# Kernel tuning notes

Measured on AMD Instinct MI355X. Metric: run time of the kernel, lower is better.

Reference implementation:

```python
import jax, jax.numpy as jnp
import numpy as np
import math

D_MODEL = 1024
N_HEADS = 16
D_HEAD = D_MODEL // N_HEADS


def setup_inputs() -> dict:
    key = jax.random.key(0)
    ks = jax.random.split(key, 9)
    B, S = 4, 2048
    scale = 1.0 / math.sqrt(D_MODEL)
    x = jax.random.normal(ks[0], (B, S, D_MODEL), dtype=jnp.float32)
    # nn.Linear weights stored as [out, in]; we keep [in, out] for x @ W
    w_q = jax.random.uniform(ks[1], (D_MODEL, D_MODEL), jnp.float32, -scale, scale)
    b_q = jax.random.uniform(ks[2], (D_MODEL,), jnp.float32, -scale, scale)
    w_k = jax.random.uniform(ks[3], (D_MODEL, D_MODEL), jnp.float32, -scale, scale)
    b_k = jax.random.uniform(ks[4], (D_MODEL,), jnp.float32, -scale, scale)
    w_v = jax.random.uniform(ks[5], (D_MODEL, D_MODEL), jnp.float32, -scale, scale)
    b_v = jax.random.uniform(ks[6], (D_MODEL,), jnp.float32, -scale, scale)
    w_o = jax.random.uniform(ks[7], (D_MODEL, D_MODEL), jnp.float32, -scale, scale)
    b_o = jax.random.uniform(ks[8], (D_MODEL,), jnp.float32, -scale, scale)
    return {"x": x, "w_q": w_q, "b_q": b_q, "w_k": w_k, "b_k": b_k,
            "w_v": w_v, "b_v": b_v, "w_o": w_o, "b_o": b_o}


def reference(x, w_q, b_q, w_k, b_k, w_v, b_v, w_o, b_o):
    B, S, _ = x.shape
    def split_heads(t):  # [B,S,D] -> [B,H,S,Dh]
        return t.reshape(B, S, N_HEADS, D_HEAD).transpose(0, 2, 1, 3)
    q = split_heads(x @ w_q + b_q)
    k = split_heads(x @ w_k + b_k)
    v = split_heads(x @ w_v + b_v)
    scores = jnp.einsum('bhqd,bhkd->bhqk', q, k) / math.sqrt(D_HEAD)
    attn = jax.nn.softmax(scores, axis=-1)  # dropout p=0 -> identity
    ctx = jnp.einsum('bhqk,bhkd->bhqd', attn, v)
    ctx = ctx.transpose(0, 2, 1, 3).reshape(B, S, D_MODEL)
    return ctx @ w_o + b_o
```

## Files before the change

kernel.cpp:

```cpp
#include <hip/hip_runtime.h>
#include <hip/hip_bf16.h>

#define DM   1024
#define SEQ  2048
#define NH   16
#define DH   64
#define BH   64
#define MTOT 8192

typedef __attribute__((ext_vector_type(8)))  short short8;
typedef __attribute__((ext_vector_type(4)))  short short4v;
typedef __attribute__((ext_vector_type(4)))  float f32x4;
typedef __attribute__((ext_vector_type(16))) float f32x16;
typedef __attribute__((ext_vector_type(4)))  float fvec4;
typedef __attribute__((ext_vector_type(4)))  int   i32x4;
typedef unsigned short ushort_t;

#define AS1 __attribute__((address_space(1)))
#define AS3 __attribute__((address_space(3)))

#define QSCALE 0.18033688011112042f
#define THR_L2 11.541560327111707f

static __device__ __forceinline__ unsigned short f2bf(float f){
  __bf16 h = (__bf16)f;
  return __builtin_bit_cast(unsigned short, h);
}

static __device__ __forceinline__ float fexp2(float x){
  float r;
  asm("v_exp_f32 %0, %1\n\ts_nop 0" : "=v"(r) : "v"(x));
  return r;
}

static __device__ __forceinline__ float fmax3(float a, float b, float c){
  float d;
  asm("v_max3_f32 %0, %1, %2, %3" : "=v"(d) : "v"(a), "v"(b), "v"(c));
  return d;
}

static __device__ __forceinline__ void gld16(const void* g, void* l){
  __builtin_amdgcn_global_load_lds((const AS1 int*)g, (AS3 int*)l, 16, 0, 0);
}

__global__ void k_cast_x(const float* __restrict__ x, ushort_t* __restrict__ xb){
  const size_t i = (size_t)blockIdx.x*256 + threadIdx.x;
  const fvec4* xv = (const fvec4*)x;
  fvec4 a = xv[2*i], b = xv[2*i+1];
  short8 r;
  #pragma unroll
  for (int j=0;j<4;++j) r[j]   = (short)f2bf(a[j]);
  #pragma unroll
  for (int j=0;j<4;++j) r[4+j] = (short)f2bf(b[j]);
  ((short8*)xb)[i] = r;
}

__global__ void k_cast_wt(const float* __restrict__ wq, const float* __restrict__ wk,
                          const float* __restrict__ wv, const float* __restrict__ wo,
                          ushort_t* __restrict__ wt){
  const int z = blockIdx.y;
  const float* W = (z==0)?wq:(z==1)?wk:(z==2)?wv:wo;
  ushort_t* Wt = wt + (size_t)z*DM*DM;
  const int k0 = (blockIdx.x & 15)*64, n0 = (blockIdx.x >> 4)*64;
  __shared__ float tile[64][65];
  const int t = threadIdx.x;
  #pragma unroll
  for (int it=0; it<4; ++it){
    int c = it*256 + t;
    int rr = c>>4, cc = c&15;
    fvec4 v = *(const fvec4*)(W + (size_t)(k0+rr)*DM + n0 + cc*4);
    #pragma unroll
    for (int j=0;j<4;++j) tile[cc*4+j][rr] = v[j];
  }
  __syncthreads();
  #pragma unroll
  for (int it=0; it<4; ++it){
    int c = it*256 + t;
    int nn = c>>4, kk = c&15;
    short4v r;
    #pragma unroll
    for (int j=0;j<4;++j) r[j] = (short)f2bf(tile[nn][kk*4+j]);
    *(short4v*)(Wt + (size_t)(n0+nn)*DM + k0 + kk*4) = r;
  }
}

template<int MODE>
__global__ __launch_bounds__(256, 2)
void k_gemm128(const ushort_t* __restrict__ A, const ushort_t* __restrict__ WtBase,
               const float* __restrict__ b0, const float* __restrict__ b1,
               const float* __restrict__ b2,
               ushort_t* __restrict__ obf, float* __restrict__ of32){
  const int z = blockIdx.z;
  const ushort_t* Wt = WtBase + (size_t)z*DM*DM;
  const float* bias = (z==0)? b0 : (z==1? b1 : b2);
  __shared__ ushort_t Al[128*32];
  __shared__ ushort_t Bl[128*32];
  const int t = threadIdx.x;
  const int wid = t>>6, l = t&63, g = l>>4, li = l&15;
  const int m0 = blockIdx.x*128, n0 = blockIdx.y*128;
  const int wr = (wid>>1)*64, wc = (wid&1)*64;
  const int srow = t>>2, schunk = (t&3)*8;

  f32x4 acc[4][4] = {};

  for (int kt = 0; kt < DM; kt += 32){
    __syncthreads();
    #pragma unroll
    for (int c = 0; c < 2; ++c){
      gld16(A  + (size_t)(m0 + c*64 + srow)*DM + kt + schunk, (char*)Al + c*4096 + wid*1024);
      gld16(Wt + (size_t)(n0 + c*64 + srow)*DM + kt + schunk, (char*)Bl + c*4096 + wid*1024);
    }
    __syncthreads();
    short8 af[4], bw[4];
    #pragma unroll
    for (int mt=0; mt<4; ++mt)
      af[mt] = *(const short8*)(Al + (wr + mt*16 + li)*32 + g*8);
    #pragma unroll
    for (int nt=0; nt<4; ++nt)
      bw[nt] = *(const short8*)(Bl + (wc + nt*16 + li)*32 + g*8);
    #pragma unroll
    for (int mt=0; mt<4; ++mt)
      #pragma unroll
      for (int nt=0; nt<4; ++nt)
        acc[mt][nt] = __builtin_amdgcn_mfma_f32_16x16x32_bf16(af[mt], bw[nt], acc[mt][nt], 0,0,0);
  }

  if constexpr (MODE==0){
    if (z == 2){
      ushort_t* vt = obf + (size_t)2*MTOT*DM;
      #pragma unroll
      for (int nt=0; nt<4; ++nt){
        const int n = n0 + wc + nt*16 + li;
        const float bn = bias[n];
        const int h = n>>6, d = n&63;
        #pragma unroll
        for (int mt=0; mt<4; ++mt){
          const int m = m0 + wr + mt*16 + g*4;
          const int bb = m >> 11, s = m & 2047;
          short4v pk;
          #pragma unroll
          for (int r=0; r<4; ++r) pk[r] = (short)f2bf(acc[mt][nt][r] + bn);
          *(short4v*)(vt + (((size_t)(bb*NH + h)*DH + d)*SEQ + s)) = pk;
        }
      }
    } else {
      const float sc = (z==0) ? QSCALE : 1.f;
      #pragma unroll
      for (int nt=0; nt<4; ++nt){
        const int n = n0 + wc + nt*16 + li;
        const float bn = bias[n];
        #pragma unroll
        for (int mt=0; mt<4; ++mt){
          #pragma unroll
          for (int r=0; r<4; ++r){
            const int m = m0 + wr + mt*16 + g*4 + r;
            const float v = (acc[mt][nt][r] + bn)*sc;
            const int bb = m >> 11, s = m & 2047, h = n >> 6, d = n & 63;
            obf[(size_t)z*MTOT*DM + (((size_t)(bb*NH + h)*SEQ + s)*DH + d)] = f2bf(v);
          }
        }
      }
    }
  } else {
    #pragma unroll
    for (int nt=0; nt<4; ++nt){
      const int n = n0 + wc + nt*16 + li;
      const float bn = bias[n];
      #pragma unroll
      for (int mt=0; mt<4; ++mt){
        #pragma unroll
        for (int r=0; r<4; ++r){
          const int m = m0 + wr + mt*16 + g*4 + r;
          of32[(size_t)m*DM + n] = acc[mt][nt][r] + bn;
        }
      }
    }
  }
}

__global__ __launch_bounds__(256, 3)
void k_attn(const ushort_t* __restrict__ Qb, const ushort_t* __restrict__ Kb,
            const ushort_t* __restrict__ Vtb, ushort_t* __restrict__ ctx){
  const int swz = (blockIdx.x & 7)*128 + (blockIdx.x >> 3);
  const int qb = swz & 15, bh = swz >> 4;
  const int b = bh>>4, h = bh&15;
  const int t = threadIdx.x, wid = t>>6, lane = t&63;
  const int lq = lane&31, hi = lane>>5;
  const int qw = qb*128 + wid*32;
  __shared__ ushort_t Kl[2][4096];
  __shared__ ushort_t Vl[2][4096];
  const ushort_t* Qh = Qb  + (size_t)bh*SEQ*DH;
  const ushort_t* Kh = Kb  + (size_t)bh*SEQ*DH;
  const ushort_t* Vh = Vtb + (size_t)bh*DH*SEQ;

  short8 qf[4];
  #pragma unroll
  for (int ks=0; ks<4; ++ks)
    qf[ks] = *(const short8*)(Qh + (size_t)(qw+lq)*DH + ks*16 + hi*8);

  f32x16 o0 = {}, o1 = {};
  f32x16 mneg16 = {};
  float ls = 0.f;

  #define STAGE(kv0, bi) do {                                              \
    _Pragma("unroll")                                                      \
    for (int i=0; i<2; ++i){                                               \
      const int c = wid*2 + i;                                             \
      gld16(Kh + (size_t)((kv0)+lane)*DH + c*8, (char*)&Kl[bi][0] + c*1024);\
      gld16(Vh + (size_t)lane*SEQ + (kv0) + c*8, (char*)&Vl[bi][0] + c*1024);\
    }                                                                      \
  } while(0)

  STAGE(0, 0);
  __syncthreads();

  int cur = 0;
  for (int t64 = 0; t64 < SEQ/64; ++t64){
    if (t64 < SEQ/64 - 1){
      if (cur) STAGE((t64+1)*64, 0); else STAGE((t64+1)*64, 1);
    }
    const char* Kb_ = (const char*)&Kl[cur][0] + hi*1024 + lq*16;
    const char* Vb_ = (const char*)&Vl[cur][0] + hi*1024 + lq*16;

    short8 kf[8];
    #pragma unroll
    for (int ks=0; ks<4; ++ks){
      kf[ks]   = *(const short8*)(Kb_ + ks*2048);
      kf[4+ks] = *(const short8*)(Kb_ + ks*2048 + 512);
    }
    f32x16 s0 = mneg16, s1 = mneg16;
    __builtin_amdgcn_s_setprio(1);
    #pragma unroll
    for (int ks=0; ks<4; ++ks){
      s0 = __builtin_amdgcn_mfma_f32_32x32x16_bf16(kf[ks],   qf[ks], s0, 0,0,0);
      s1 = __builtin_amdgcn_mfma_f32_32x32x16_bf16(kf[4+ks], qf[ks], s1, 0,0,0);
    }
    __builtin_amdgcn_s_setprio(0);

    float mx[8];
    #pragma unroll
    for (int i=0;i<8;++i) mx[i] = fmax3(s0[i], s0[8+i], s1[i]);
    float y0 = fmax3(mx[0], mx[4], s1[8]);
    float y1 = fmax3(mx[1], mx[5], s1[9]);
    float y2 = fmax3(mx[2], mx[6], s1[10]);
    float y3 = fmax3(mx[3], mx[7], s1[11]);
    float z0 = fmax3(y0, y1, s1[12]);
    float z1 = fmax3(y2, y3, s1[13]);
    float tm = fmax3(fmax3(z0, z1, s1[14]), s1[15], -1e30f);
    tm = fmaxf(tm, __shfl_xor(tm, 32));

    if (!__all(tm <= THR_L2)){
      const float tmx = fmaxf(tm, 0.f);
      const float fac = fexp2(-tmx);
      ls *= fac;
      #pragma unroll
      for (int r=0; r<16; ++r){
        const float fr = __shfl(fac, (r&3) + 8*(r>>2) + 4*hi);
        o0[r] *= fr; o1[r] *= fr;
      }
      #pragma unroll
      for (int r=0; r<16; ++r){ s0[r] -= tmx; s1[r] -= tmx; mneg16[r] -= tmx; }
    }

    float ps[4] = {0.f, 0.f, 0.f, 0.f};
    #pragma unroll
    for (int r=0; r<16; ++r){ float e = fexp2(s0[r]); s0[r]=e; ps[r&3]+=e; }
    #pragma unroll
    for (int r=0; r<16; ++r){ float e = fexp2(s1[r]); s1[r]=e; ps[r&3]+=e; }
    ls += (ps[0]+ps[1]) + (ps[2]+ps[3]);

    short8 pa[4];
    #pragma unroll
    for (int blk=0; blk<2; ++blk){
      #pragma unroll
      for (int half=0; half<2; ++half){
        i32x4 w;
        #pragma unroll
        for (int wp=0; wp<2; ++wp){
          const int base = half*8 + 2*wp;
          float a0 = blk ? s1[base]   : s0[base];
          float a1 = blk ? s1[base+1] : s0[base+1];
          float c0 = blk ? s1[base+4] : s0[base+4];
          float c1 = blk ? s1[base+5] : s0[base+5];
          int x, y;
          asm("v_cvt_pk_bf16_f32 %0, %1, %2" : "=v"(x) : "v"(a0), "v"(a1));
          asm("v_cvt_pk_bf16_f32 %0, %1, %2" : "=v"(y) : "v"(c0), "v"(c1));
          asm("v_permlane32_swap_b32 %0, %1" : "+v"(x), "+v"(y));
          w[wp] = x; w[2+wp] = y;
        }
        pa[blk*2+half] = __builtin_bit_cast(short8, w);
      }
    }

    short8 vb[8];
    #pragma unroll
    for (int ks=0; ks<4; ++ks){
      vb[ks]   = *(const short8*)(Vb_ + ks*2048);
      vb[4+ks] = *(const short8*)(Vb_ + ks*2048 + 512);
    }
    __builtin_amdgcn_s_setprio(1);
    #pragma unroll
    for (int ks=0; ks<4; ++ks){
      o0 = __builtin_amdgcn_mfma_f32_32x32x16_bf16(pa[ks], vb[ks],   o0, 0,0,0);
      o1 = __builtin_amdgcn_mfma_f32_32x32x16_bf16(pa[ks], vb[4+ks], o1, 0,0,0);
    }
    __builtin_amdgcn_s_setprio(0);

    __syncthreads();
    cur ^= 1;
  }

  ls += __shfl_xor(ls, 32);
  const float inv = 1.f / ls;
  #pragma unroll
  for (int r=0; r<16; ++r){
    const float iv = __shfl(inv, (r&3) + 8*(r>>2) + 4*hi);
    const int qrow = qw + (r&3) + 8*(r>>2) + 4*hi;
    ushort_t* dst = ctx + ((size_t)(b*SEQ + qrow))*DM + h*DH;
    dst[lq]    = f2bf(o0[r]*iv);
    dst[32+lq] = f2bf(o1[r]*iv);
  }
  #undef STAGE
}

extern "C" void kernel_launch(void* const* d_in, const int* in_sizes, int n_in,
                              void* d_out, int out_size, void* d_ws, size_t ws_size,
                              hipStream_t stream){
  const float* x  = (const float*)d_in[0];
  const float* wq = (const float*)d_in[1];
  const float* bq = (const float*)d_in[2];
  const float* wk = (const float*)d_in[3];
  const float* bk = (const float*)d_in[4];
  const float* wv = (const float*)d_in[5];
  const float* bv = (const float*)d_in[6];
  const float* wo = (const float*)d_in[7];
  const float* bo = (const float*)d_in[8];
  float* out = (float*)d_out;

  ushort_t* xb  = (ushort_t*)d_ws;
  ushort_t* wt  = xb  + (size_t)MTOT*DM;
  ushort_t* qkv = wt  + (size_t)4*DM*DM;
  ushort_t* ctx = qkv + (size_t)3*MTOT*DM;

  k_cast_x<<<4096, 256, 0, stream>>>(x, xb);
  k_cast_wt<<<dim3(256,4), 256, 0, stream>>>(wq, wk, wv, wo, wt);
  k_gemm128<0><<<dim3(64,8,3), 256, 0, stream>>>(xb, wt, bq, bk, bv, qkv, nullptr);
  k_attn<<<1024, 256, 0, stream>>>(qkv, qkv + (size_t)MTOT*DM, qkv + (size_t)2*MTOT*DM, ctx);
  k_gemm128<1><<<dim3(64,8,1), 256, 0, stream>>>(ctx, wt + (size_t)3*DM*DM, bo, bo, bo, nullptr, out);
}
```

Measured before the change: 282.4 us.

## Stage Q tile in LDS, pack softmax sum adds, flatten QKV GEMM grid

```diff
diff --git a/kernel.cpp b/kernel.cpp
--- a/kernel.cpp
+++ b/kernel.cpp
@@ -11,6 +11,7 @@
 typedef __attribute__((ext_vector_type(8)))  short short8;
 typedef __attribute__((ext_vector_type(4)))  short short4v;
 typedef __attribute__((ext_vector_type(4)))  float f32x4;
+typedef __attribute__((ext_vector_type(2)))  float f32x2;
 typedef __attribute__((ext_vector_type(16))) float f32x16;
 typedef __attribute__((ext_vector_type(4)))  float fvec4;
 typedef __attribute__((ext_vector_type(4)))  int   i32x4;
@@ -29,13 +30,19 @@
 
 static __device__ __forceinline__ float fexp2(float x){
   float r;
-  asm("v_exp_f32 %0, %1\n\ts_nop 0" : "=v"(r) : "v"(x));
+  asm("v_exp_f32 %0, %1" : "=v"(r) : "v"(x));
   return r;
 }
 
 static __device__ __forceinline__ float fmax3(float a, float b, float c){
   float d;
   asm("v_max3_f32 %0, %1, %2, %3" : "=v"(d) : "v"(a), "v"(b), "v"(c));
+  return d;
+}
+
+static __device__ __forceinline__ f32x2 pkadd(f32x2 a, f32x2 b){
+  f32x2 d;
+  asm("v_pk_add_f32 %0, %1, %2" : "=v"(d) : "v"(a), "v"(b));
   return d;
 }
 
@@ -90,14 +97,16 @@
                const float* __restrict__ b0, const float* __restrict__ b1,
                const float* __restrict__ b2,
                ushort_t* __restrict__ obf, float* __restrict__ of32){
-  const int z = blockIdx.z;
+  const int by = blockIdx.y;
+  const int z  = (MODE==0) ? (by>>3) : 0;
+  const int n0 = (MODE==0) ? ((by&7)*128) : by*128;
   const ushort_t* Wt = WtBase + (size_t)z*DM*DM;
   const float* bias = (z==0)? b0 : (z==1? b1 : b2);
   __shared__ ushort_t Al[128*32];
   __shared__ ushort_t Bl[128*32];
   const int t = threadIdx.x;
   const int wid = t>>6, l = t&63, g = l>>4, li = l&15;
-  const int m0 = blockIdx.x*128, n0 = blockIdx.y*128;
+  const int m0 = blockIdx.x*128;
   const int wr = (wid>>1)*64, wc = (wid&1)*64;
   const int srow = t>>2, schunk = (t&3)*8;
 
@@ -186,17 +195,21 @@
   const int b = bh>>4, h = bh&15;
   const int t = threadIdx.x, wid = t>>6, lane = t&63;
   const int lq = lane&31, hi = lane>>5;
-  const int qw = qb*128 + wid*32;
+  __shared__ ushort_t Ql[8192];
   __shared__ ushort_t Kl[2][4096];
   __shared__ ushort_t Vl[2][4096];
   const ushort_t* Qh = Qb  + (size_t)bh*SEQ*DH;
   const ushort_t* Kh = Kb  + (size_t)bh*SEQ*DH;
   const ushort_t* Vh = Vtb + (size_t)bh*DH*SEQ;
 
-  short8 qf[4];
-  #pragma unroll
-  for (int ks=0; ks<4; ++ks)
-    qf[ks] = *(const short8*)(Qh + (size_t)(qw+lq)*DH + ks*16 + hi*8);
+  #pragma unroll
+  for (int i=0; i<2; ++i){
+    const int c = wid*2 + i;
+    #pragma unroll
+    for (int half=0; half<2; ++half)
+      gld16(Qh + (size_t)(qb*128 + half*64 + lane)*DH + c*8,
+            (char*)Ql + c*2048 + half*1024);
+  }
 
   f32x16 o0 = {}, o1 = {};
   f32x16 mneg16 = {};
@@ -214,6 +227,8 @@
   STAGE(0, 0);
   __syncthreads();
 
+  const char* Qp = (const char*)Ql + hi*2048 + (wid*32 + lq)*16;
+
   int cur = 0;
   for (int t64 = 0; t64 < SEQ/64; ++t64){
     if (t64 < SEQ/64 - 1){
@@ -221,6 +236,11 @@
     }
     const char* Kb_ = (const char*)&Kl[cur][0] + hi*1024 + lq*16;
     const char* Vb_ = (const char*)&Vl[cur][0] + hi*1024 + lq*16;
+
+    short8 qf[4];
+    #pragma unroll
+    for (int ks=0; ks<4; ++ks)
+      qf[ks] = *(const short8*)(Qp + ks*4096);
 
     short8 kf[8];
     #pragma unroll
@@ -246,7 +266,7 @@
     float y3 = fmax3(mx[3], mx[7], s1[11]);
     float z0 = fmax3(y0, y1, s1[12]);
     float z1 = fmax3(y2, y3, s1[13]);
-    float tm = fmax3(fmax3(z0, z1, s1[14]), s1[15], -1e30f);
+    float tm = fmaxf(fmax3(z0, z1, s1[14]), s1[15]);
     tm = fmaxf(tm, __shfl_xor(tm, 32));
 
     if (!__all(tm <= THR_L2)){
@@ -262,12 +282,18 @@
       for (int r=0; r<16; ++r){ s0[r] -= tmx; s1[r] -= tmx; mneg16[r] -= tmx; }
     }
 
-    float ps[4] = {0.f, 0.f, 0.f, 0.f};
-    #pragma unroll
-    for (int r=0; r<16; ++r){ float e = fexp2(s0[r]); s0[r]=e; ps[r&3]+=e; }
-    #pragma unroll
-    for (int r=0; r<16; ++r){ float e = fexp2(s1[r]); s1[r]=e; ps[r&3]+=e; }
-    ls += (ps[0]+ps[1]) + (ps[2]+ps[3]);
+    #pragma unroll
+    for (int r=0; r<16; ++r) s0[r] = fexp2(s0[r]);
+    #pragma unroll
+    for (int r=0; r<16; ++r) s1[r] = fexp2(s1[r]);
+    f32x2 ac = {0.f, 0.f};
+    #pragma unroll
+    for (int r=0; r<16; r+=4){
+      f32x2 u = pkadd(f32x2{s0[r], s0[r+1]}, f32x2{s0[r+2], s0[r+3]});
+      f32x2 v = pkadd(f32x2{s1[r], s1[r+1]}, f32x2{s1[r+2], s1[r+3]});
+      ac = pkadd(ac, pkadd(u, v));
+    }
+    ls += ac[0] + ac[1];
 
     short8 pa[4];
     #pragma unroll
@@ -312,6 +338,7 @@
 
   ls += __shfl_xor(ls, 32);
   const float inv = 1.f / ls;
+  const int qw = qb*128 + wid*32;
   #pragma unroll
   for (int r=0; r<16; ++r){
     const float iv = __shfl(inv, (r&3) + 8*(r>>2) + 4*hi);
@@ -344,7 +371,7 @@
 
   k_cast_x<<<4096, 256, 0, stream>>>(x, xb);
   k_cast_wt<<<dim3(256,4), 256, 0, stream>>>(wq, wk, wv, wo, wt);
-  k_gemm128<0><<<dim3(64,8,3), 256, 0, stream>>>(xb, wt, bq, bk, bv, qkv, nullptr);
+  k_gemm128<0><<<dim3(64,24), 256, 0, stream>>>(xb, wt, bq, bk, bv, qkv, nullptr);
   k_attn<<<1024, 256, 0, stream>>>(qkv, qkv + (size_t)MTOT*DM, qkv + (size_t)2*MTOT*DM, ctx);
-  k_gemm128<1><<<dim3(64,8,1), 256, 0, stream>>>(ctx, wt + (size_t)3*DM*DM, bo, bo, bo, nullptr, out);
-}
+  k_gemm128<1><<<dim3(64,8), 256, 0, stream>>>(ctx, wt + (size_t)3*DM*DM, bo, bo, bo, nullptr, out);
+}
```

Result: no change. 280.7 us (-0.6%).
